# Performance work log

Measured on AMD Instinct MI355X. Metric: run time of the kernel, lower is better.

Reference implementation:

```python
import jax, jax.numpy as jnp
import numpy as np

DIM = 768
NUM_EXPERTS = 4
NUM_HEADS = 12
HEAD_DIM = DIM // NUM_HEADS
MLP_HID = 4 * DIM
FC1_OUT = MLP_HID + 3 * DIM   # 5376 (mlp hidden + qkv)
FC2_IN = MLP_HID + DIM        # 3840 (mlp hidden + attn out)
FC2_OUT = 2 * DIM             # 1536 (mlp out + attn proj out)
CAP_FACTOR = 0.5
LN_EPS = 1e-6


def setup_inputs() -> dict:
    key = jax.random.key(0)
    ks = jax.random.split(key, 4)
    B, N = 8, 1024
    return {
        "x": jax.random.normal(ks[0], (B, N, DIM), jnp.float32),
        "w_router": jax.random.normal(ks[1], (NUM_EXPERTS, DIM), jnp.float32) * 0.02,
        "gamma1": jnp.ones((DIM,), jnp.float32),
        "beta1": jnp.zeros((DIM,), jnp.float32),
        "w1": jax.random.normal(ks[2], (FC1_OUT, DIM), jnp.float32) * 0.02,
        "b1": jnp.zeros((FC1_OUT,), jnp.float32),
        "w2": jax.random.normal(ks[3], (FC2_OUT, FC2_IN), jnp.float32) * 0.02,
        "b2": jnp.zeros((FC2_OUT,), jnp.float32),
    }


def reference(x, w_router, gamma1, beta1, w1, b1, w2, b2):
    B, N, C = x.shape
    E = NUM_EXPERTS
    cap = int(CAP_FACTOR * N)
    # nested (MoNE) per-expert active dims: [96, 192, 384, 768] for E=4, C=768
    m = np.array([C // 2 ** (E - 1 - e) for e in range(E)])
    in_mask = (np.arange(C)[None, :] < m[:, None]).astype(np.float32)  # [E, C]
    in_mask = jnp.asarray(in_mask)
    out_mask = jnp.concatenate([in_mask, in_mask], axis=-1)  # [E, 2C] for fc2 chunks

    # ---- expert-choice router ----
    logits = jnp.einsum('bnc,ec->bne', x, w_router)          # [B, N, E]
    probs = jax.nn.softmax(logits, axis=-1)
    gate, idx = jax.lax.top_k(jnp.swapaxes(probs, 1, 2), cap)  # [B, E, cap]
    dispatch = jax.nn.one_hot(idx, N, dtype=x.dtype)           # [B, E, cap, N]
    combine = dispatch * gate[..., None]                       # [B, E, cap, N]

    # ---- norm1 ----
    mu = jnp.mean(x, -1, keepdims=True)
    var = jnp.var(x, -1, keepdims=True)
    y = (x - mu) * jax.lax.rsqrt(var + LN_EPS) * gamma1 + beta1

    # ---- experts_choose_masked_contract (fc1, nested input dims) ----
    xg = jnp.einsum('becn,bnd->becd', dispatch, y)             # gather [B,E,cap,C]
    xg = xg * in_mask[None, :, None, :]                        # nested expert slice
    h = jnp.einsum('becd,fd->becf', xg, w1) + b1               # [B,E,cap,FC1_OUT]
    h = jnp.einsum('becn,becf->bnf', dispatch, h)              # scatter [B,N,FC1_OUT]

    x_mlp, x_qkv = h[..., :MLP_HID], h[..., MLP_HID:]

    # ---- attention ----
    qkv = x_qkv.reshape(B, N, 3, NUM_HEADS, HEAD_DIM).transpose(2, 0, 3, 1, 4)
    q, k, v = qkv[0], qkv[1], qkv[2]                           # [B,H,N,hd]
    scale = HEAD_DIM ** -0.5
    attn = jax.nn.softmax(jnp.einsum('bhqd,bhkd->bhqk', q, k) * scale, axis=-1)
    x_attn = jnp.einsum('bhqk,bhkd->bhqd', attn, v)
    x_attn = x_attn.transpose(0, 2, 1, 3).reshape(B, N, C)

    # ---- mlp activation + concat ----
    x_mlp = jax.nn.gelu(x_mlp, approximate=False)
    y2 = jnp.concatenate([x_mlp, x_attn], axis=-1)             # [B,N,FC2_IN]

    # ---- experts_choose_masked_expand (fc2, nested output dims, combine-weighted) ----
    yg = jnp.einsum('becn,bnf->becf', dispatch, y2)            # gather [B,E,cap,FC2_IN]
    o = jnp.einsum('becf,of->beco', yg, w2) + b2               # [B,E,cap,FC2_OUT]
    o = o * out_mask[None, :, None, :]                         # nested expert output slice
    z = jnp.einsum('becn,beco->bno', combine, o)               # combine [B,N,FC2_OUT]

    x_mlp2, x_attn2 = z[..., :C], z[..., C:]
    return x + x_mlp2 + x_attn2
```

## Files before the change

### kernel.cpp

```cpp
#include <hip/hip_runtime.h>
#include <math.h>

typedef __bf16 bf16_t;
typedef __bf16 bf16x8 __attribute__((ext_vector_type(8)));
typedef __bf16 bf16x4 __attribute__((ext_vector_type(4)));
typedef float f32x4 __attribute__((ext_vector_type(4)));

#define DIM 768
#define NE 4
#define NH 12
#define HD 64
#define MLP_HID 3072
#define FC1_OUT 5376
#define FC2_IN 3840
#define CAP 512
#define LOG2E 1.44269504088896340736f

__device__ __forceinline__ void async_copy16(const void* g, void* l) {
  __builtin_amdgcn_global_load_lds((const __attribute__((address_space(1))) void*)g,
                                   (__attribute__((address_space(3))) void*)l, 16, 0, 0);
}

__device__ __forceinline__ float gelu_f(float v) {
  float v2 = v * v;
  float t = v * fmaf(-0.102944f, v2, -2.302208f);
  float e = exp2f(t);
  return v * __builtin_amdgcn_rcpf(1.0f + e);
}

__global__ __launch_bounds__(256) void cast_router_kernel(const float* __restrict__ w1,
                                                          const float* __restrict__ w2,
                                                          bf16_t* __restrict__ w1b,
                                                          bf16_t* __restrict__ w2b,
                                                          const float* __restrict__ x,
                                                          const float* __restrict__ wr,
                                                          float* __restrict__ probs) {
  if (blockIdx.x < 2048) {
    const int N1 = FC1_OUT * DIM;
    const int N2 = 1536 * FC2_IN;
    for (int i = blockIdx.x * 256 + threadIdx.x; i < N1 + N2; i += 2048 * 256) {
      if (i < N1) w1b[i] = (bf16_t)w1[i];
      else        w2b[i - N1] = (bf16_t)w2[i - N1];
    }
    return;
  }
  int t = (blockIdx.x - 2048) * 4 + (threadIdx.x >> 6);
  int l = threadIdx.x & 63;
  const float* xr = x + (size_t)t * DIM;
  float a0 = 0.f, a1 = 0.f, a2 = 0.f, a3 = 0.f;
#pragma unroll
  for (int i = 0; i < 12; i++) {
    int d = l + i * 64;
    float xv = xr[d];
    a0 += xv * wr[d];
    a1 += xv * wr[DIM + d];
    a2 += xv * wr[2 * DIM + d];
    a3 += xv * wr[3 * DIM + d];
  }
#pragma unroll
  for (int off = 32; off > 0; off >>= 1) {
    a0 += __shfl_down(a0, off);
    a1 += __shfl_down(a1, off);
    a2 += __shfl_down(a2, off);
    a3 += __shfl_down(a3, off);
  }
  if (l == 0) {
    float m = fmaxf(fmaxf(a0, a1), fmaxf(a2, a3));
    float e0 = expf(a0 - m), e1 = expf(a1 - m), e2 = expf(a2 - m), e3 = expf(a3 - m);
    float inv = 1.0f / (e0 + e1 + e2 + e3);
    int b = t >> 10, n = t & 1023;
    probs[(b * NE + 0) * 1024 + n] = e0 * inv;
    probs[(b * NE + 1) * 1024 + n] = e1 * inv;
    probs[(b * NE + 2) * 1024 + n] = e2 * inv;
    probs[(b * NE + 3) * 1024 + n] = e3 * inv;
  }
}

__global__ __launch_bounds__(256) void rank_kernel(const float* __restrict__ probs,
                                                   float* __restrict__ gate_tok) {
  int be = blockIdx.y;
  __shared__ float p[1024];
  for (int i = threadIdx.x; i < 1024; i += 256) p[i] = probs[be * 1024 + i];
  __syncthreads();
  int n = blockIdx.x * 256 + threadIdx.x;
  float pn = p[n];
  int rank = 0;
  for (int j = 0; j < 1024; j++) {
    float pj = p[j];
    rank += (pj > pn) || (pj == pn && j < n);
  }
  int b = be >> 2, e = be & 3;
  gate_tok[(size_t)((b << 10) + n) * 4 + e] = (rank < CAP) ? pn : 0.0f;
}

__global__ __launch_bounds__(256) void ln_kernel(const float* __restrict__ x,
                                                 const float* __restrict__ gamma,
                                                 const float* __restrict__ beta,
                                                 const float* __restrict__ gate_tok,
                                                 bf16_t* __restrict__ ytil,
                                                 float* __restrict__ cntf,
                                                 float* __restrict__ g4) {
  int t = blockIdx.x * 4 + (threadIdx.x >> 6);
  int l = threadIdx.x & 63;
  float4 gg = ((const float4*)gate_tok)[t];
  float s0 = (gg.x > 0.f) ? 1.f : 0.f;
  float s1 = (gg.y > 0.f) ? 1.f : 0.f;
  float s2 = (gg.z > 0.f) ? 1.f : 0.f;
  float s3 = (gg.w > 0.f) ? 1.f : 0.f;
  float c3 = s3, c2 = c3 + s2, c1 = c2 + s1, c0 = c1 + s0;
  if (l == 0) {
    cntf[t] = c0;
    float4 G;
    G.x = gg.x + gg.y + gg.z + gg.w;
    G.y = gg.y + gg.z + gg.w;
    G.z = gg.z + gg.w;
    G.w = gg.w;
    ((float4*)g4)[t] = G;
  }
  const float* xr = x + (size_t)t * DIM;
  float v[12];
  float s = 0.f, sq = 0.f;
#pragma unroll
  for (int i = 0; i < 12; i++) {
    v[i] = xr[l + i * 64];
    s += v[i];
    sq += v[i] * v[i];
  }
#pragma unroll
  for (int off = 1; off < 64; off <<= 1) {
    s += __shfl_xor(s, off);
    sq += __shfl_xor(sq, off);
  }
  float mean = s * (1.0f / DIM);
  float var = sq * (1.0f / DIM) - mean * mean;
  float rs = rsqrtf(var + 1e-6f);
#pragma unroll
  for (int i = 0; i < 12; i++) {
    int d = l + i * 64;
    float cf = (d < 96) ? c0 : (d < 192) ? c1 : (d < 384) ? c2 : c3;
    ytil[(size_t)t * DIM + d] = (bf16_t)(((v[i] - mean) * rs * gamma[d] + beta[d]) * cf);
  }
}

__global__ __launch_bounds__(256, 4) void fc1_kernel(const bf16_t* __restrict__ ytil,
                                                     const bf16_t* __restrict__ w1b,
                                                     const float* __restrict__ b1,
                                                     const float* __restrict__ cntf,
                                                     bf16_t* __restrict__ y2b,
                                                     bf16_t* __restrict__ qb,
                                                     bf16_t* __restrict__ kb,
                                                     bf16_t* __restrict__ vtb) {
  const int bid = blockIdx.x;
  const int xcd = bid & 7, j = bid >> 3;
  const int mt = xcd * 8 + (j & 7);
  const int nt = j >> 3;
  const int tid = threadIdx.x;
  const int w = tid >> 6, l = tid & 63;
  const int lq = l >> 4, lr = l & 15;

  __shared__ __align__(16) bf16_t lA[128 * 64];
  __shared__ __align__(16) bf16_t lB[128 * 64];

  f32x4 acc[4][4] = {};
  const int mwave = (w & 1) * 64, nwave = (w >> 1) * 64;
  const int crow = l >> 3;
  const int cbg = (l & 7) ^ (crow & 7);

  for (int k0 = 0; k0 < DIM; k0 += 64) {
#pragma unroll
    for (int i = 0; i < 4; i++) {
      int c = w * 4 + i;
      int row = c * 8 + crow;
      async_copy16(ytil + (size_t)(mt * 128 + row) * DIM + k0 + cbg * 8, lA + c * 512);
      async_copy16(w1b + (size_t)(nt * 128 + row) * DIM + k0 + cbg * 8, lB + c * 512);
    }
    __syncthreads();
#pragma unroll
    for (int ks = 0; ks < 2; ks++) {
      const int cbA = ((ks * 4 + lq) ^ (lr & 7)) * 8;
      bf16x8 af[4], bfr[4];
#pragma unroll
      for (int mi = 0; mi < 4; mi++)
        af[mi] = *(const bf16x8*)(lA + (mwave + mi * 16 + lr) * 64 + cbA);
#pragma unroll
      for (int ni = 0; ni < 4; ni++)
        bfr[ni] = *(const bf16x8*)(lB + (nwave + ni * 16 + lr) * 64 + cbA);
#pragma unroll
      for (int mi = 0; mi < 4; mi++)
#pragma unroll
        for (int ni = 0; ni < 4; ni++)
          acc[mi][ni] = __builtin_amdgcn_mfma_f32_16x16x32_bf16(af[mi], bfr[ni], acc[mi][ni], 0, 0, 0);
    }
    __syncthreads();
  }

#pragma unroll
  for (int mi = 0; mi < 4; mi++) {
    int row0 = mt * 128 + mwave + mi * 16 + lq * 4;
    float cnt[4];
#pragma unroll
    for (int r = 0; r < 4; r++) cnt[r] = cntf[row0 + r];
#pragma unroll
    for (int ni = 0; ni < 4; ni++) {
      int col = nt * 128 + nwave + ni * 16 + lr;
      float bias = b1[col];
      if (col < MLP_HID) {
#pragma unroll
        for (int r = 0; r < 4; r++) {
          float v = acc[mi][ni][r] + cnt[r] * bias;
          y2b[(size_t)(row0 + r) * FC2_IN + col] = (bf16_t)gelu_f(v);
        }
      } else {
        int part = col - MLP_HID;
        int comp = (part >= 1536) ? 2 : (part >= 768) ? 1 : 0;
        int rem = part - comp * 768;
        int hh = rem >> 6, d = rem & 63;
        int b = row0 >> 10, n0 = row0 & 1023;
        size_t base = (size_t)(b * NH + hh);
        if (comp == 2) {
          bf16x4 pk;
#pragma unroll
          for (int r = 0; r < 4; r++)
            pk[r] = (bf16_t)(acc[mi][ni][r] + cnt[r] * bias);
          *(bf16x4*)(vtb + (base * HD + d) * 1024 + n0) = pk;
        } else {
#pragma unroll
          for (int r = 0; r < 4; r++) {
            float v = acc[mi][ni][r] + cnt[r] * bias;
            if (comp == 0) qb[(base * 1024 + n0 + r) * HD + d] = (bf16_t)(v * (0.125f * LOG2E));
            else           kb[(base * 1024 + n0 + r) * HD + d] = (bf16_t)v;
          }
        }
      }
    }
  }
}

__global__ __launch_bounds__(256) void attn_kernel(const bf16_t* __restrict__ qb,
                                                   const bf16_t* __restrict__ kb,
                                                   const bf16_t* __restrict__ vtb,
                                                   bf16_t* __restrict__ y2b) {
  const int bid = blockIdx.x;
  const int xcd = bid & 7, j = bid >> 3;
  const int bh = xcd * 12 + (j >> 3);
  const int qt = j & 7;
  const int tid = threadIdx.x;
  const int w = tid >> 6, l = tid & 63, lq = l >> 4, lr = l & 15;

  __shared__ __align__(16) bf16_t lK[64 * 64];
  __shared__ __align__(16) bf16_t lV[64 * 64];
  __shared__ __align__(16) bf16_t lP[4][16 * 72];

  const bf16_t* qbase = qb + (size_t)bh * 1024 * HD;
  const bf16_t* kbase = kb + (size_t)bh * 1024 * HD;
  const bf16_t* vbase = vtb + (size_t)bh * HD * 1024;

  bf16x8 qf[2][2];
#pragma unroll
  for (int h = 0; h < 2; h++) {
    int qrow = qt * 128 + h * 64 + w * 16 + lr;
#pragma unroll
    for (int s = 0; s < 2; s++)
      qf[h][s] = *(const bf16x8*)(qbase + (size_t)qrow * HD + s * 32 + lq * 8);
  }

  f32x4 oacc[2][4] = {};
  float psum[2][4] = {};

  const int crow = l >> 3;
  const int cbg = (l & 7) ^ (crow & 7);

  for (int kt = 0; kt < 16; kt++) {
#pragma unroll
    for (int i = 0; i < 2; i++) {
      int c = w * 2 + i;
      int row = c * 8 + crow;
      async_copy16(kbase + (size_t)(kt * 64 + row) * HD + cbg * 8, lK + c * 512);
      async_copy16(vbase + (size_t)row * 1024 + kt * 64 + cbg * 8, lV + c * 512);
    }
    __syncthreads();

#pragma unroll
    for (int h = 0; h < 2; h++) {
      f32x4 sacc[4] = {};
#pragma unroll
      for (int s = 0; s < 2; s++) {
        const int cb = ((s * 4 + lq) ^ (lr & 7)) * 8;
#pragma unroll
        for (int kbq = 0; kbq < 4; kbq++) {
          bf16x8 kf = *(const bf16x8*)(lK + (kbq * 16 + lr) * 64 + cb);
          sacc[kbq] = __builtin_amdgcn_mfma_f32_16x16x32_bf16(qf[h][s], kf, sacc[kbq], 0, 0, 0);
        }
      }

#pragma unroll
      for (int kbq = 0; kbq < 4; kbq++)
#pragma unroll
        for (int r = 0; r < 4; r++) {
          float pv = exp2f(sacc[kbq][r]);
          psum[h][r] += pv;
          lP[w][(lq * 4 + r) * 72 + kbq * 16 + lr] = (bf16_t)pv;
        }

      bf16x8 pf[2];
#pragma unroll
      for (int s = 0; s < 2; s++)
        pf[s] = *(const bf16x8*)(&lP[w][lr * 72 + s * 32 + lq * 8]);

#pragma unroll
      for (int s = 0; s < 2; s++) {
        const int cb = ((s * 4 + lq) ^ (lr & 7)) * 8;
#pragma unroll
        for (int nb = 0; nb < 4; nb++) {
          bf16x8 vf = *(const bf16x8*)(lV + (nb * 16 + lr) * 64 + cb);
          oacc[h][nb] = __builtin_amdgcn_mfma_f32_16x16x32_bf16(pf[s], vf, oacc[h][nb], 0, 0, 0);
        }
      }
    }
    __syncthreads();
  }

  int b = bh / NH, hh = bh % NH;
#pragma unroll
  for (int h = 0; h < 2; h++) {
#pragma unroll
    for (int off = 1; off < 16; off <<= 1)
#pragma unroll
      for (int r = 0; r < 4; r++) psum[h][r] += __shfl_xor(psum[h][r], off);
    float rinv[4];
#pragma unroll
    for (int r = 0; r < 4; r++) rinv[r] = 1.0f / psum[h][r];
#pragma unroll
    for (int nb = 0; nb < 4; nb++)
#pragma unroll
      for (int r = 0; r < 4; r++) {
        float v = oacc[h][nb][r] * rinv[r];
        int tok = qt * 128 + h * 64 + w * 16 + lq * 4 + r;
        y2b[((size_t)(b * 1024 + tok)) * FC2_IN + MLP_HID + hh * HD + nb * 16 + lr] = (bf16_t)v;
      }
  }
}

__global__ __launch_bounds__(512, 2) void fc2_kernel(const bf16_t* __restrict__ y2b,
                                                     const bf16_t* __restrict__ w2b,
                                                     const float* __restrict__ b2,
                                                     const float* __restrict__ g4,
                                                     const float* __restrict__ x,
                                                     float* __restrict__ out) {
  const int bid = blockIdx.x;
  const int xcd = bid & 7, j = bid >> 3;
  const int mt = xcd * 4 + (j >> 3);
  const int ct = j & 7;
  const int tid = threadIdx.x;
  const int w = tid >> 6, l = tid & 63;
  const int lq = l >> 4, lr = l & 15;
  const int wm = w & 1, wn = w >> 1;

  __shared__ __align__(16) bf16_t lA[2][256 * 64];
  __shared__ __align__(16) bf16_t lB[2][192 * 64];

  f32x4 acc[8][3] = {};
  const int crow = l >> 3;
  const int cbg = (l & 7) ^ (crow & 7);

  auto stage = [&](int buf, int k0) {
#pragma unroll
    for (int i = 0; i < 4; i++) {
      int c = w * 4 + i;
      int row = c * 8 + crow;
      async_copy16(y2b + (size_t)(mt * 256 + row) * FC2_IN + k0 + cbg * 8, &lA[buf][c * 512]);
    }
#pragma unroll
    for (int i = 0; i < 3; i++) {
      int c = w * 3 + i;
      int r = c * 8 + crow;
      int grow = (r & 1) * 768 + ct * 96 + (r >> 1);
      async_copy16(w2b + (size_t)grow * FC2_IN + k0 + cbg * 8, &lB[buf][c * 512]);
    }
  };

  auto compute = [&](int buf) {
    const bf16_t* la = lA[buf];
    const bf16_t* lb = lB[buf];
    __builtin_amdgcn_s_setprio(1);
#pragma unroll
    for (int ks = 0; ks < 2; ks++) {
      const int cb = ((ks * 4 + lq) ^ (lr & 7)) * 8;
      bf16x8 af[8], bfr[3];
#pragma unroll
      for (int mi = 0; mi < 8; mi++)
        af[mi] = *(const bf16x8*)(la + (wm * 128 + mi * 16 + lr) * 64 + cb);
#pragma unroll
      for (int ni = 0; ni < 3; ni++)
        bfr[ni] = *(const bf16x8*)(lb + (wn * 48 + ni * 16 + lr) * 64 + cb);
#pragma unroll
      for (int mi = 0; mi < 8; mi++)
#pragma unroll
        for (int ni = 0; ni < 3; ni++)
          acc[mi][ni] = __builtin_amdgcn_mfma_f32_16x16x32_bf16(af[mi], bfr[ni], acc[mi][ni], 0, 0, 0);
    }
    __builtin_amdgcn_s_setprio(0);
  };

  stage(0, 0);
  stage(1, 64);
  asm volatile("s_waitcnt vmcnt(7)" ::: "memory");
  __builtin_amdgcn_s_barrier();
  __builtin_amdgcn_sched_barrier(0);

  int cur = 0;
  for (int kt = 0; kt < 58; ++kt) {
    compute(cur);
    asm volatile("s_waitcnt lgkmcnt(0)" ::: "memory");
    __builtin_amdgcn_sched_barrier(0);
    __builtin_amdgcn_s_barrier();
    __builtin_amdgcn_sched_barrier(0);
    stage(cur, (kt + 2) * 64);
    asm volatile("s_waitcnt vmcnt(7)" ::: "memory");
    __builtin_amdgcn_s_barrier();
    __builtin_amdgcn_sched_barrier(0);
    cur ^= 1;
  }
  compute(cur);
  asm volatile("s_waitcnt vmcnt(0)" ::: "memory");
  __builtin_amdgcn_s_barrier();
  __builtin_amdgcn_sched_barrier(0);
  compute(cur ^ 1);

  const int row_base = mt * 256 + wm * 128;
#pragma unroll
  for (int mi = 0; mi < 8; mi++) {
    const int row0 = row_base + mi * 16 + lq * 4;
    float4 G[4];
#pragma unroll
    for (int r = 0; r < 4; r++) G[r] = ((const float4*)g4)[row0 + r];
#pragma unroll
    for (int ni = 0; ni < 3; ni++) {
      const int col = ct * 96 + wn * 24 + ni * 8 + (lr >> 1);
      const float bh = b2[(lr & 1) * 768 + col];
#pragma unroll
      for (int r = 0; r < 4; r++) {
        float s = acc[mi][ni][r] + bh;
        s += __shfl_xor(s, 1);
        if (!(lr & 1)) {
          float gw = (col < 96) ? G[r].x : (col < 192) ? G[r].y : (col < 384) ? G[r].z : G[r].w;
          size_t idx = (size_t)(row0 + r) * DIM + col;
          out[idx] = x[idx] + gw * s;
        }
      }
    }
  }
}

extern "C" void kernel_launch(void* const* d_in, const int* in_sizes, int n_in,
                              void* d_out, int out_size, void* d_ws, size_t ws_size,
                              hipStream_t stream) {
  const float* x     = (const float*)d_in[0];
  const float* wr    = (const float*)d_in[1];
  const float* gamma = (const float*)d_in[2];
  const float* beta  = (const float*)d_in[3];
  const float* w1    = (const float*)d_in[4];
  const float* b1    = (const float*)d_in[5];
  const float* w2    = (const float*)d_in[6];
  const float* b2    = (const float*)d_in[7];
  float* out = (float*)d_out;

  char* ws = (char*)d_ws;
  float*  probs    = (float*)(ws + 0);
  float*  gate_tok = (float*)(ws + 131072);
  float*  cntf     = (float*)(ws + 262144);
  float*  g4       = (float*)(ws + 294912);
  bf16_t* w1b      = (bf16_t*)(ws + 425984);
  bf16_t* w2b      = (bf16_t*)(ws + 8683520);
  bf16_t* ytil     = (bf16_t*)(ws + 20480000);
  bf16_t* y2b      = (bf16_t*)(ws + 33062912);
  bf16_t* qb       = (bf16_t*)(ws + 95977472);
  bf16_t* kb       = (bf16_t*)(ws + 108560384);
  bf16_t* vtb      = (bf16_t*)(ws + 121143296);

  cast_router_kernel<<<4096, 256, 0, stream>>>(w1, w2, w1b, w2b, x, wr, probs);
  rank_kernel<<<dim3(4, 32), 256, 0, stream>>>(probs, gate_tok);
  ln_kernel<<<2048, 256, 0, stream>>>(x, gamma, beta, gate_tok, ytil, cntf, g4);
  fc1_kernel<<<2688, 256, 0, stream>>>(ytil, w1b, b1, cntf, y2b, qb, kb, vtb);
  attn_kernel<<<768, 256, 0, stream>>>(qb, kb, vtb, y2b);
  fc2_kernel<<<256, 512, 0, stream>>>(y2b, w2b, b2, g4, x, out);
}
```

Baseline: 394.9 us.

## Retile fc2 GEMM to 128x384 tiles with split-K half-stage pipelining

```diff
diff --git a/kernel.cpp b/kernel.cpp
--- a/kernel.cpp
+++ b/kernel.cpp
@@ -349,94 +349,114 @@
                                                      float* __restrict__ out) {
   const int bid = blockIdx.x;
   const int xcd = bid & 7, j = bid >> 3;
-  const int mt = xcd * 4 + (j >> 3);
-  const int ct = j & 7;
+  const int mt = xcd * 8 + (j >> 2);
+  const int nt = j & 3;
   const int tid = threadIdx.x;
   const int w = tid >> 6, l = tid & 63;
   const int lq = l >> 4, lr = l & 15;
   const int wm = w & 1, wn = w >> 1;
 
-  __shared__ __align__(16) bf16_t lA[2][256 * 64];
-  __shared__ __align__(16) bf16_t lB[2][192 * 64];
-
-  f32x4 acc[8][3] = {};
-  const int crow = l >> 3;
-  const int cbg = (l & 7) ^ (crow & 7);
-
-  auto stage = [&](int buf, int k0) {
-#pragma unroll
-    for (int i = 0; i < 4; i++) {
-      int c = w * 4 + i;
-      int row = c * 8 + crow;
-      async_copy16(y2b + (size_t)(mt * 256 + row) * FC2_IN + k0 + cbg * 8, &lA[buf][c * 512]);
-    }
-#pragma unroll
-    for (int i = 0; i < 3; i++) {
-      int c = w * 3 + i;
-      int r = c * 8 + crow;
-      int grow = (r & 1) * 768 + ct * 96 + (r >> 1);
-      async_copy16(w2b + (size_t)grow * FC2_IN + k0 + cbg * 8, &lB[buf][c * 512]);
-    }
+  __shared__ __align__(16) bf16_t lA[2][2][128 * 32];
+  __shared__ __align__(16) bf16_t lB[2][2][384 * 32];
+
+  f32x4 acc[4][6] = {};
+
+  const int srow = w * 16 + (l >> 2);
+  const int sk8 = (((l & 3) ^ ((l >> 3) & 3)) * 8);
+  const bf16_t* aSrc = y2b + (size_t)(mt * 128 + srow) * FC2_IN + sk8;
+  const bf16_t* bSrc0;
+  const bf16_t* bSrc1;
+  const bf16_t* bSrc2;
+  {
+    int bn0 = 0 * 128 + srow, bn1 = 1 * 128 + srow, bn2 = 2 * 128 + srow;
+    bSrc0 = w2b + (size_t)((bn0 & 1) * 768 + nt * 192 + (bn0 >> 1)) * FC2_IN + sk8;
+    bSrc1 = w2b + (size_t)((bn1 & 1) * 768 + nt * 192 + (bn1 >> 1)) * FC2_IN + sk8;
+    bSrc2 = w2b + (size_t)((bn2 & 1) * 768 + nt * 192 + (bn2 >> 1)) * FC2_IN + sk8;
+  }
+  const int rsw = (lq ^ ((lr >> 1) & 3)) * 8;
+
+  auto stageA = [&](int buf, int h, int t) {
+    async_copy16(aSrc + t * 64 + h * 32, &lA[buf][h][w * 512]);
   };
-
-  auto compute = [&](int buf) {
-    const bf16_t* la = lA[buf];
-    const bf16_t* lb = lB[buf];
+  auto stageB = [&](int buf, int h, int t) {
+    async_copy16(bSrc0 + t * 64 + h * 32, &lB[buf][h][0 * 4096 + w * 512]);
+    async_copy16(bSrc1 + t * 64 + h * 32, &lB[buf][h][1 * 4096 + w * 512]);
+    async_copy16(bSrc2 + t * 64 + h * 32, &lB[buf][h][2 * 4096 + w * 512]);
+  };
+  auto readA = [&](bf16x8* af, int buf, int h) {
+#pragma unroll
+    for (int mi = 0; mi < 4; mi++)
+      af[mi] = *(const bf16x8*)(&lA[buf][h][(wm * 64 + mi * 16 + lr) * 32 + rsw]);
+  };
+  auto readB = [&](bf16x8* bf, int buf, int h, int nb) {
+#pragma unroll
+    for (int k = 0; k < 3; k++)
+      bf[k] = *(const bf16x8*)(&lB[buf][h][(wn * 96 + (nb + k) * 16 + lr) * 32 + rsw]);
+  };
+  auto domfma = [&](bf16x8* af, bf16x8* bf, int nb) {
     __builtin_amdgcn_s_setprio(1);
 #pragma unroll
-    for (int ks = 0; ks < 2; ks++) {
-      const int cb = ((ks * 4 + lq) ^ (lr & 7)) * 8;
-      bf16x8 af[8], bfr[3];
-#pragma unroll
-      for (int mi = 0; mi < 8; mi++)
-        af[mi] = *(const bf16x8*)(la + (wm * 128 + mi * 16 + lr) * 64 + cb);
-#pragma unroll
-      for (int ni = 0; ni < 3; ni++)
-        bfr[ni] = *(const bf16x8*)(lb + (wn * 48 + ni * 16 + lr) * 64 + cb);
-#pragma unroll
-      for (int mi = 0; mi < 8; mi++)
-#pragma unroll
-        for (int ni = 0; ni < 3; ni++)
-          acc[mi][ni] = __builtin_amdgcn_mfma_f32_16x16x32_bf16(af[mi], bfr[ni], acc[mi][ni], 0, 0, 0);
-    }
+    for (int mi = 0; mi < 4; mi++)
+#pragma unroll
+      for (int k = 0; k < 3; k++)
+        acc[mi][nb + k] = __builtin_amdgcn_mfma_f32_16x16x32_bf16(af[mi], bf[k], acc[mi][nb + k], 0, 0, 0);
     __builtin_amdgcn_s_setprio(0);
   };
 
-  stage(0, 0);
-  stage(1, 64);
-  asm volatile("s_waitcnt vmcnt(7)" ::: "memory");
+  stageA(0, 0, 0); stageB(0, 0, 0); stageA(0, 1, 0); stageB(0, 1, 0);
+  stageA(1, 0, 1); stageB(1, 0, 1); stageA(1, 1, 1);
+  asm volatile("s_waitcnt vmcnt(5)" ::: "memory");
   __builtin_amdgcn_s_barrier();
   __builtin_amdgcn_sched_barrier(0);
 
-  int cur = 0;
-  for (int kt = 0; kt < 58; ++kt) {
-    compute(cur);
+  const int NT = FC2_IN / 64;
+  for (int t = 0; t < NT; ++t) {
+    const int buf = t & 1;
+    bf16x8 a0[4], a1[4], bfrag[3];
+    readA(a0, buf, 0);
+    readB(bfrag, buf, 0, 0);
+    if (t + 1 < NT) stageB(buf ^ 1, 1, t + 1);
+    __builtin_amdgcn_s_barrier();
     asm volatile("s_waitcnt lgkmcnt(0)" ::: "memory");
     __builtin_amdgcn_sched_barrier(0);
-    __builtin_amdgcn_s_barrier();
+    domfma(a0, bfrag, 0);
+    __builtin_amdgcn_s_barrier();
+    readB(bfrag, buf, 0, 3);
+    if (t + 2 < NT) stageA(buf, 0, t + 2);
+    __builtin_amdgcn_s_barrier();
+    asm volatile("s_waitcnt lgkmcnt(0)" ::: "memory");
     __builtin_amdgcn_sched_barrier(0);
-    stage(cur, (kt + 2) * 64);
-    asm volatile("s_waitcnt vmcnt(7)" ::: "memory");
-    __builtin_amdgcn_s_barrier();
+    domfma(a0, bfrag, 3);
+    __builtin_amdgcn_s_barrier();
+    readA(a1, buf, 1);
+    readB(bfrag, buf, 1, 0);
+    if (t + 2 < NT) stageB(buf, 0, t + 2);
+    __builtin_amdgcn_s_barrier();
+    asm volatile("s_waitcnt lgkmcnt(0)" ::: "memory");
     __builtin_amdgcn_sched_barrier(0);
-    cur ^= 1;
-  }
-  compute(cur);
-  asm volatile("s_waitcnt vmcnt(0)" ::: "memory");
-  __builtin_amdgcn_s_barrier();
-  __builtin_amdgcn_sched_barrier(0);
-  compute(cur ^ 1);
-
-  const int row_base = mt * 256 + wm * 128;
-#pragma unroll
-  for (int mi = 0; mi < 8; mi++) {
-    const int row0 = row_base + mi * 16 + lq * 4;
+    domfma(a1, bfrag, 0);
+    __builtin_amdgcn_s_barrier();
+    readB(bfrag, buf, 1, 3);
+    if (t + 2 < NT) stageA(buf, 1, t + 2);
+    __builtin_amdgcn_s_barrier();
+    asm volatile("s_waitcnt lgkmcnt(0)" ::: "memory");
+    __builtin_amdgcn_sched_barrier(0);
+    domfma(a1, bfrag, 3);
+    asm volatile("s_waitcnt vmcnt(5)" ::: "memory");
+    __builtin_amdgcn_s_barrier();
+    __builtin_amdgcn_sched_barrier(0);
+  }
+
+  const int rowb = mt * 128 + wm * 64;
+#pragma unroll
+  for (int mi = 0; mi < 4; mi++) {
+    const int row0 = rowb + mi * 16 + lq * 4;
     float4 G[4];
 #pragma unroll
     for (int r = 0; r < 4; r++) G[r] = ((const float4*)g4)[row0 + r];
 #pragma unroll
-    for (int ni = 0; ni < 3; ni++) {
-      const int col = ct * 96 + wn * 24 + ni * 8 + (lr >> 1);
+    for (int ni = 0; ni < 6; ni++) {
+      const int col = nt * 192 + wn * 48 + ni * 8 + (lr >> 1);
       const float bh = b2[(lr & 1) * 768 + col];
 #pragma unroll
       for (int r = 0; r < 4; r++) {
```

Result: slower. 433.4 us (+9.7%).
